# Performance work log

Hardware: AMD Instinct MI355X
Metric: run time of the kernel (lower is better)

The kernel has to match this reference:

```python
import jax, jax.numpy as jnp
import numpy as np

B, L, D = 32, 2048, 768
H = 512
EPS = 1e-5  # batch_norm eps (PyG MLP default norm)


def setup_inputs() -> dict:
    key = jax.random.key(0)
    ks = jax.random.split(key, 8)
    hidden = jax.random.normal(ks[0], (B, L, D), dtype=jnp.float32)
    attention_mask = jax.random.randint(ks[1], (B, L), 0, 2, dtype=jnp.int32)
    W1 = jax.random.normal(ks[2], (D, H), dtype=jnp.float32) * 0.02
    b1 = jnp.zeros((H,), dtype=jnp.float32)
    gamma = jnp.ones((H,), dtype=jnp.float32)
    beta = jnp.zeros((H,), dtype=jnp.float32)
    W2 = jax.random.normal(ks[3], (H, H), dtype=jnp.float32) * 0.02
    b2 = jnp.zeros((H,), dtype=jnp.float32)
    return {"hidden": hidden, "attention_mask": attention_mask,
            "W1": W1, "b1": b1, "gamma": gamma, "beta": beta,
            "W2": W2, "b2": b2}


def reference(hidden, attention_mask, W1, b1, gamma, beta, W2, b2):
    # Valid-token mask; pads are excluded from the batched graph's node set.
    m = attention_mask.astype(hidden.dtype)[..., None]  # (B, L, 1)
    n_valid = jnp.maximum(jnp.sum(m), 1.0)

    # MLP layer 1: Linear -> BatchNorm (stats over all valid nodes across the
    # whole batched graph, mirroring PyG MLP training-mode batch_norm) -> ReLU
    h = jnp.einsum('bld,dh->blh', hidden, W1) + b1  # (B, L, H)
    mean = jnp.sum(h * m, axis=(0, 1)) / n_valid
    var = jnp.sum(jnp.square(h - mean) * m, axis=(0, 1)) / n_valid
    h = (h - mean) * jax.lax.rsqrt(var + EPS) * gamma + beta
    h = jax.nn.relu(h)

    # MLP layer 2 (plain_last: no norm/act)
    out = jnp.einsum('blh,hk->blk', h, W2) + b2  # (B, L, H)

    # scores == ones -> segment softmax over each sequence's valid tokens is
    # uniform 1/n_b; scatter_add over batch ids == masked mean pool.
    counts = jnp.maximum(jnp.sum(m, axis=1), 1.0)  # (B, 1)
    pooled = jnp.sum(out * m, axis=1) / counts  # (B, H)
    return pooled
```

## Files before the change

### kernel.cpp

```cpp
#include <hip/hip_runtime.h>
#include <hip/hip_bf16.h>

#define Bn 32
#define Ln 2048
#define Dn 768
#define Hn 512
#define Mn (Bn*Ln)
#define EPSC 1e-5f

#define OFF_S1   0
#define OFF_S2   512
#define OFF_SC   1024
#define OFF_SH   1536
#define OFF_CNT  2048
#define OFF_PH   2304
#define ZERO_N   (OFF_PH + Bn*Hn)
#define OFF_W1T_BYTES  131072
#define OFF_H_BYTES    1048576

#define BM 128
#define BN2 256
#define BK 64
#define LDK 72

typedef __attribute__((ext_vector_type(8))) short bf16x8;
typedef __attribute__((ext_vector_type(4))) float f32x4;

static __device__ __forceinline__ unsigned short f2bf(float x) {
  __hip_bfloat16 h = __float2bfloat16(x);
  return *reinterpret_cast<unsigned short*>(&h);
}
static __device__ __forceinline__ float bf2f(unsigned short u) {
  return __uint_as_float(((unsigned int)u) << 16);
}

__global__ void zero_kernel(float* __restrict__ p, int n) {
  int i = blockIdx.x * 256 + threadIdx.x;
  if (i < n) p[i] = 0.f;
}

__global__ void count_kernel(const int* __restrict__ mask, float* __restrict__ cnt) {
  __shared__ int red[256];
  int b = blockIdx.x, t = threadIdx.x;
  int s = 0;
#pragma unroll
  for (int i = 0; i < 8; i++) s += mask[b * Ln + i * 256 + t];
  red[t] = s;
  __syncthreads();
  for (int off = 128; off > 0; off >>= 1) {
    if (t < off) red[t] += red[t + off];
    __syncthreads();
  }
  if (t == 0) cnt[b] = (float)red[0];
}

__global__ __launch_bounds__(256) void transpose_w1(
    const float* __restrict__ W1, unsigned short* __restrict__ W1t) {
  __shared__ float tile[32][33];
  int kx = blockIdx.x * 32;
  int nx = blockIdx.y * 32;
  int tx = threadIdx.x & 31, ty = threadIdx.x >> 5;
#pragma unroll
  for (int i = 0; i < 32; i += 8)
    tile[ty + i][tx] = W1[(size_t)(kx + ty + i) * Hn + nx + tx];
  __syncthreads();
#pragma unroll
  for (int i = 0; i < 32; i += 8)
    W1t[(size_t)(nx + ty + i) * Dn + kx + tx] = f2bf(tile[tx][ty + i]);
}

__global__ __launch_bounds__(512, 4) void gemm1_mfma(
    const float* __restrict__ A, const unsigned short* __restrict__ W1t,
    const float* __restrict__ b1, const int* __restrict__ mask,
    unsigned short* __restrict__ Hout,
    float* __restrict__ gsum, float* __restrict__ gsq)
{
  __shared__ unsigned short As[BM * LDK];
  __shared__ unsigned short Bs[BN2 * LDK];
  __shared__ float csum[BN2];
  __shared__ float csq[BN2];

  const int t = threadIdx.x;
  const int bx = blockIdx.x;
  const int by = blockIdx.y;
  const int bm0 = by * BM;
  const int bn0 = bx * BN2;

  const int w = t >> 6;
  const int lane = t & 63;
  const int wm0 = (w >> 2) * 64;
  const int wn0 = (w & 3) * 64;
  const int l15 = lane & 15;
  const int quad = lane >> 4;

  const int am = t >> 2;
  const int ak = (t & 3) * 16;
  const int bn = t >> 1;
  const int bk = (t & 1) * 32;

  const float* Ap = A + (size_t)(bm0 + am) * Dn + ak;
  const unsigned short* Bp = W1t + (size_t)(bn0 + bn) * Dn + bk;

  f32x4 acc[4][4];
#pragma unroll
  for (int i = 0; i < 4; i++)
#pragma unroll
    for (int j = 0; j < 4; j++) acc[i][j] = (f32x4){0.f, 0.f, 0.f, 0.f};

  for (int k0 = 0; k0 < Dn; k0 += BK) {
    float4 a0 = *(const float4*)(Ap + k0);
    float4 a1 = *(const float4*)(Ap + k0 + 4);
    float4 a2 = *(const float4*)(Ap + k0 + 8);
    float4 a3 = *(const float4*)(Ap + k0 + 12);
    uint4 bv0 = *(const uint4*)(Bp + k0);
    uint4 bv1 = *(const uint4*)(Bp + k0 + 8);
    uint4 bv2 = *(const uint4*)(Bp + k0 + 16);
    uint4 bv3 = *(const uint4*)(Bp + k0 + 24);
    __syncthreads();
    uint4 p0, p1;
    p0.x = (unsigned int)f2bf(a0.x) | ((unsigned int)f2bf(a0.y) << 16);
    p0.y = (unsigned int)f2bf(a0.z) | ((unsigned int)f2bf(a0.w) << 16);
    p0.z = (unsigned int)f2bf(a1.x) | ((unsigned int)f2bf(a1.y) << 16);
    p0.w = (unsigned int)f2bf(a1.z) | ((unsigned int)f2bf(a1.w) << 16);
    p1.x = (unsigned int)f2bf(a2.x) | ((unsigned int)f2bf(a2.y) << 16);
    p1.y = (unsigned int)f2bf(a2.z) | ((unsigned int)f2bf(a2.w) << 16);
    p1.z = (unsigned int)f2bf(a3.x) | ((unsigned int)f2bf(a3.y) << 16);
    p1.w = (unsigned int)f2bf(a3.z) | ((unsigned int)f2bf(a3.w) << 16);
    *(uint4*)&As[am * LDK + ak] = p0;
    *(uint4*)&As[am * LDK + ak + 8] = p1;
    *(uint4*)&Bs[bn * LDK + bk] = bv0;
    *(uint4*)&Bs[bn * LDK + bk + 8] = bv1;
    *(uint4*)&Bs[bn * LDK + bk + 16] = bv2;
    *(uint4*)&Bs[bn * LDK + bk + 24] = bv3;
    __syncthreads();
#pragma unroll
    for (int s = 0; s < 2; s++) {
      bf16x8 af[4], bf[4];
#pragma unroll
      for (int mt = 0; mt < 4; mt++)
        af[mt] = *(const bf16x8*)&As[(wm0 + mt * 16 + l15) * LDK + s * 32 + quad * 8];
#pragma unroll
      for (int nt = 0; nt < 4; nt++)
        bf[nt] = *(const bf16x8*)&Bs[(wn0 + nt * 16 + l15) * LDK + s * 32 + quad * 8];
#pragma unroll
      for (int mt = 0; mt < 4; mt++)
#pragma unroll
        for (int nt = 0; nt < 4; nt++)
          acc[mt][nt] = __builtin_amdgcn_mfma_f32_16x16x32_bf16(
              af[mt], bf[nt], acc[mt][nt], 0, 0, 0);
    }
  }

  if (t < BN2) { csum[t] = 0.f; csq[t] = 0.f; }
  __syncthreads();

  float mk[4][4];
#pragma unroll
  for (int mt = 0; mt < 4; mt++) {
    int4 mv = *(const int4*)(mask + bm0 + wm0 + mt * 16 + quad * 4);
    mk[mt][0] = (float)mv.x; mk[mt][1] = (float)mv.y;
    mk[mt][2] = (float)mv.z; mk[mt][3] = (float)mv.w;
  }

  const size_t cbase = ((size_t)(by * 2 + bx)) * 32768 + (size_t)w * 4096;
#pragma unroll
  for (int nt = 0; nt < 4; nt++) {
    const int nl = wn0 + nt * 16 + l15;
    const float bias = b1[bn0 + nl];
    float ps = 0.f, pq = 0.f;
#pragma unroll
    for (int mt = 0; mt < 4; mt++) {
      ushort4 st;
      float v0 = acc[mt][nt][0] + bias;
      float v1 = acc[mt][nt][1] + bias;
      float v2 = acc[mt][nt][2] + bias;
      float v3 = acc[mt][nt][3] + bias;
      ps += v0 * mk[mt][0] + v1 * mk[mt][1] + v2 * mk[mt][2] + v3 * mk[mt][3];
      pq += v0 * v0 * mk[mt][0] + v1 * v1 * mk[mt][1] +
            v2 * v2 * mk[mt][2] + v3 * v3 * mk[mt][3];
      st.x = f2bf(v0); st.y = f2bf(v1); st.z = f2bf(v2); st.w = f2bf(v3);
      *(ushort4*)&Hout[cbase + (size_t)(mt * 4 + nt) * 256 + lane * 4] = st;
    }
    atomicAdd(&csum[nl], ps);
    atomicAdd(&csq[nl], pq);
  }

  __syncthreads();
  if (t < BN2) {
    atomicAdd(&gsum[bn0 + t], csum[t]);
    atomicAdd(&gsq[bn0 + t], csq[t]);
  }
}

__global__ void finalize_kernel(float* __restrict__ ws,
                                const float* __restrict__ gamma,
                                const float* __restrict__ beta) {
  __shared__ float nv;
  int t = threadIdx.x;
  if (t == 0) {
    float s = 0.f;
    for (int i = 0; i < Bn; i++) s += ws[OFF_CNT + i];
    nv = fmaxf(s, 1.f);
  }
  __syncthreads();
  float inv = 1.f / nv;
  float m = ws[OFF_S1 + t] * inv;
  float var = ws[OFF_S2 + t] * inv - m * m;
  float istd = rsqrtf(fmaxf(var, 0.f) + EPSC);
  float sc = istd * gamma[t];
  ws[OFF_SC + t] = sc;
  ws[OFF_SH + t] = beta[t] - m * sc;
}

__global__ __launch_bounds__(256) void bnpool_kernel(
    const unsigned short* __restrict__ Hbuf, const int* __restrict__ mask,
    const float* __restrict__ sc, const float* __restrict__ sh,
    float* __restrict__ pooled)
{
  __shared__ float pool_c[BN2];
  __shared__ float mkf[BM];
  __shared__ float scs[BN2], shs[BN2];
  const int t = threadIdx.x;
  const int chunk = blockIdx.x;
  const int by = chunk >> 1, bx = chunk & 1;
  const int b = by >> 4;
  pool_c[t] = 0.f;
  if (t < BM) mkf[t] = (float)mask[by * BM + t];
  scs[t] = sc[bx * BN2 + t];
  shs[t] = sh[bx * BN2 + t];
  __syncthreads();
  const unsigned short* base = Hbuf + (size_t)chunk * 32768;
#pragma unroll 4
  for (int i = 0; i < 32; i++) {
    int o = (i * 256 + t) * 4;
    ushort4 hv = *(const ushort4*)(base + o);
    int lane = (o >> 2) & 63;
    int mtnt = (o >> 8) & 15;
    int w = o >> 12;
    int nl = (w & 3) * 64 + (mtnt & 3) * 16 + (lane & 15);
    int ml = (w >> 2) * 64 + (mtnt >> 2) * 16 + (lane >> 4) * 4;
    float4 mv = *(const float4*)&mkf[ml];
    float scv = scs[nl], shv = shs[nl];
    float s = 0.f;
    s = fmaf(fmaxf(fmaf(bf2f(hv.x), scv, shv), 0.f), mv.x, s);
    s = fmaf(fmaxf(fmaf(bf2f(hv.y), scv, shv), 0.f), mv.y, s);
    s = fmaf(fmaxf(fmaf(bf2f(hv.z), scv, shv), 0.f), mv.z, s);
    s = fmaf(fmaxf(fmaf(bf2f(hv.w), scv, shv), 0.f), mv.w, s);
    atomicAdd(&pool_c[nl], s);
  }
  __syncthreads();
  atomicAdd(&pooled[b * Hn + bx * BN2 + t], pool_c[t]);
}

__global__ __launch_bounds__(128) void final_kernel(
    const float* __restrict__ pooledh, const float* __restrict__ cnt,
    const float* __restrict__ W2, const float* __restrict__ b2,
    float* __restrict__ out)
{
  __shared__ float pr[Hn];
  int b = blockIdx.x >> 2;
  int cc = blockIdx.x & 3;
  int t = threadIdx.x;
  float nb = cnt[b];
  float inv = 1.f / fmaxf(nb, 1.f);
#pragma unroll
  for (int i = 0; i < 4; i++)
    pr[t + i * 128] = pooledh[b * Hn + t + i * 128] * inv;
  __syncthreads();
  int c = cc * 128 + t;
  float a = 0.f;
  for (int i = 0; i < Hn; i++)
    a = fmaf(pr[i], W2[(size_t)i * Hn + c], a);
  out[b * Hn + c] = a + b2[c] * (nb * inv);
}

extern "C" void kernel_launch(void* const* d_in, const int* in_sizes, int n_in,
                              void* d_out, int out_size, void* d_ws, size_t ws_size,
                              hipStream_t stream) {
  const float* hidden = (const float*)d_in[0];
  const int*   mask   = (const int*)d_in[1];
  const float* W1     = (const float*)d_in[2];
  const float* b1     = (const float*)d_in[3];
  const float* gamma  = (const float*)d_in[4];
  const float* beta   = (const float*)d_in[5];
  const float* W2     = (const float*)d_in[6];
  const float* b2     = (const float*)d_in[7];
  float* out = (float*)d_out;
  float* ws  = (float*)d_ws;
  unsigned short* W1t  = (unsigned short*)((char*)d_ws + OFF_W1T_BYTES);
  unsigned short* Hbuf = (unsigned short*)((char*)d_ws + OFF_H_BYTES);

  zero_kernel<<<(ZERO_N + 255) / 256, 256, 0, stream>>>(ws, ZERO_N);
  count_kernel<<<Bn, 256, 0, stream>>>(mask, ws + OFF_CNT);
  transpose_w1<<<dim3(Dn / 32, Hn / 32), 256, 0, stream>>>(W1, W1t);
  gemm1_mfma<<<dim3(Hn / BN2, Mn / BM), 512, 0, stream>>>(
      hidden, W1t, b1, mask, Hbuf, ws + OFF_S1, ws + OFF_S2);
  finalize_kernel<<<1, Hn, 0, stream>>>(ws, gamma, beta);
  bnpool_kernel<<<(Mn / BM) * (Hn / BN2), 256, 0, stream>>>(
      Hbuf, mask, ws + OFF_SC, ws + OFF_SH, ws + OFF_PH);
  final_kernel<<<Bn * 4, 128, 0, stream>>>(ws + OFF_PH, ws + OFF_CNT, W2, b2, out);
}
```

Measured before the change: 421.7 us.

## Prefetch GEMM tiles, store H column-major per chunk, atomic-free pooling per channel

Register-prefetches the next K slice of A and B in the GEMM main loop so global loads overlap the MFMA work. Changes the bf16 H intermediate layout to channel-major within each 128-row chunk, and rewrites the BN+ReLU+pool kernel to run one block per channel. Each block reduces all batches with warp shuffles and writes without atomics, which also lets the zeroing kernel skip the pooled buffer. The final matvec is split into four independent accumulators. Risks include higher register pressure in the GEMM and strided, less-coalesced reads in the pool kernel.

```diff
diff --git a/kernel.cpp b/kernel.cpp
--- a/kernel.cpp
+++ b/kernel.cpp
@@ -14,7 +14,7 @@
 #define OFF_SH   1536
 #define OFF_CNT  2048
 #define OFF_PH   2304
-#define ZERO_N   (OFF_PH + Bn*Hn)
+#define ZERO_N   1024
 #define OFF_W1T_BYTES  131072
 #define OFF_H_BYTES    1048576
 
@@ -107,32 +107,45 @@
 #pragma unroll
     for (int j = 0; j < 4; j++) acc[i][j] = (f32x4){0.f, 0.f, 0.f, 0.f};
 
+  float4 ra0 = *(const float4*)(Ap);
+  float4 ra1 = *(const float4*)(Ap + 4);
+  float4 ra2 = *(const float4*)(Ap + 8);
+  float4 ra3 = *(const float4*)(Ap + 12);
+  uint4 rb0 = *(const uint4*)(Bp);
+  uint4 rb1 = *(const uint4*)(Bp + 8);
+  uint4 rb2 = *(const uint4*)(Bp + 16);
+  uint4 rb3 = *(const uint4*)(Bp + 24);
+
   for (int k0 = 0; k0 < Dn; k0 += BK) {
-    float4 a0 = *(const float4*)(Ap + k0);
-    float4 a1 = *(const float4*)(Ap + k0 + 4);
-    float4 a2 = *(const float4*)(Ap + k0 + 8);
-    float4 a3 = *(const float4*)(Ap + k0 + 12);
-    uint4 bv0 = *(const uint4*)(Bp + k0);
-    uint4 bv1 = *(const uint4*)(Bp + k0 + 8);
-    uint4 bv2 = *(const uint4*)(Bp + k0 + 16);
-    uint4 bv3 = *(const uint4*)(Bp + k0 + 24);
     __syncthreads();
     uint4 p0, p1;
-    p0.x = (unsigned int)f2bf(a0.x) | ((unsigned int)f2bf(a0.y) << 16);
-    p0.y = (unsigned int)f2bf(a0.z) | ((unsigned int)f2bf(a0.w) << 16);
-    p0.z = (unsigned int)f2bf(a1.x) | ((unsigned int)f2bf(a1.y) << 16);
-    p0.w = (unsigned int)f2bf(a1.z) | ((unsigned int)f2bf(a1.w) << 16);
-    p1.x = (unsigned int)f2bf(a2.x) | ((unsigned int)f2bf(a2.y) << 16);
-    p1.y = (unsigned int)f2bf(a2.z) | ((unsigned int)f2bf(a2.w) << 16);
-    p1.z = (unsigned int)f2bf(a3.x) | ((unsigned int)f2bf(a3.y) << 16);
-    p1.w = (unsigned int)f2bf(a3.z) | ((unsigned int)f2bf(a3.w) << 16);
+    p0.x = (unsigned int)f2bf(ra0.x) | ((unsigned int)f2bf(ra0.y) << 16);
+    p0.y = (unsigned int)f2bf(ra0.z) | ((unsigned int)f2bf(ra0.w) << 16);
+    p0.z = (unsigned int)f2bf(ra1.x) | ((unsigned int)f2bf(ra1.y) << 16);
+    p0.w = (unsigned int)f2bf(ra1.z) | ((unsigned int)f2bf(ra1.w) << 16);
+    p1.x = (unsigned int)f2bf(ra2.x) | ((unsigned int)f2bf(ra2.y) << 16);
+    p1.y = (unsigned int)f2bf(ra2.z) | ((unsigned int)f2bf(ra2.w) << 16);
+    p1.z = (unsigned int)f2bf(ra3.x) | ((unsigned int)f2bf(ra3.y) << 16);
+    p1.w = (unsigned int)f2bf(ra3.z) | ((unsigned int)f2bf(ra3.w) << 16);
     *(uint4*)&As[am * LDK + ak] = p0;
     *(uint4*)&As[am * LDK + ak + 8] = p1;
-    *(uint4*)&Bs[bn * LDK + bk] = bv0;
-    *(uint4*)&Bs[bn * LDK + bk + 8] = bv1;
-    *(uint4*)&Bs[bn * LDK + bk + 16] = bv2;
-    *(uint4*)&Bs[bn * LDK + bk + 24] = bv3;
+    *(uint4*)&Bs[bn * LDK + bk] = rb0;
+    *(uint4*)&Bs[bn * LDK + bk + 8] = rb1;
+    *(uint4*)&Bs[bn * LDK + bk + 16] = rb2;
+    *(uint4*)&Bs[bn * LDK + bk + 24] = rb3;
     __syncthreads();
+
+    if (k0 + BK < Dn) {
+      ra0 = *(const float4*)(Ap + k0 + BK);
+      ra1 = *(const float4*)(Ap + k0 + BK + 4);
+      ra2 = *(const float4*)(Ap + k0 + BK + 8);
+      ra3 = *(const float4*)(Ap + k0 + BK + 12);
+      rb0 = *(const uint4*)(Bp + k0 + BK);
+      rb1 = *(const uint4*)(Bp + k0 + BK + 8);
+      rb2 = *(const uint4*)(Bp + k0 + BK + 16);
+      rb3 = *(const uint4*)(Bp + k0 + BK + 24);
+    }
+
 #pragma unroll
     for (int s = 0; s < 2; s++) {
       bf16x8 af[4], bf[4];
@@ -162,7 +175,7 @@
     mk[mt][2] = (float)mv.z; mk[mt][3] = (float)mv.w;
   }
 
-  const size_t cbase = ((size_t)(by * 2 + bx)) * 32768 + (size_t)w * 4096;
+  const size_t cbase = ((size_t)(by * 2 + bx)) * 32768;
 #pragma unroll
   for (int nt = 0; nt < 4; nt++) {
     const int nl = wn0 + nt * 16 + l15;
@@ -179,7 +192,7 @@
       pq += v0 * v0 * mk[mt][0] + v1 * v1 * mk[mt][1] +
             v2 * v2 * mk[mt][2] + v3 * v3 * mk[mt][3];
       st.x = f2bf(v0); st.y = f2bf(v1); st.z = f2bf(v2); st.w = f2bf(v3);
-      *(ushort4*)&Hout[cbase + (size_t)(mt * 4 + nt) * 256 + lane * 4] = st;
+      *(ushort4*)&Hout[cbase + (size_t)nl * 128 + wm0 + mt * 16 + quad * 4] = st;
     }
     atomicAdd(&csum[nl], ps);
     atomicAdd(&csq[nl], pq);
@@ -217,39 +230,41 @@
     const float* __restrict__ sc, const float* __restrict__ sh,
     float* __restrict__ pooled)
 {
-  __shared__ float pool_c[BN2];
-  __shared__ float mkf[BM];
-  __shared__ float scs[BN2], shs[BN2];
+  __shared__ float part[4][32];
   const int t = threadIdx.x;
-  const int chunk = blockIdx.x;
-  const int by = chunk >> 1, bx = chunk & 1;
-  const int b = by >> 4;
-  pool_c[t] = 0.f;
-  if (t < BM) mkf[t] = (float)mask[by * BM + t];
-  scs[t] = sc[bx * BN2 + t];
-  shs[t] = sh[bx * BN2 + t];
-  __syncthreads();
-  const unsigned short* base = Hbuf + (size_t)chunk * 32768;
+  const int c = blockIdx.x;
+  const int bx = c >> 8, cl = c & 255;
+  const int w4 = t >> 6, lane = t & 63;
+  const float scv = sc[c], shv = sh[c];
+
+  float acc[32];
+#pragma unroll
+  for (int j = 0; j < 32; j++) acc[j] = 0.f;
+
 #pragma unroll 4
-  for (int i = 0; i < 32; i++) {
-    int o = (i * 256 + t) * 4;
-    ushort4 hv = *(const ushort4*)(base + o);
-    int lane = (o >> 2) & 63;
-    int mtnt = (o >> 8) & 15;
-    int w = o >> 12;
-    int nl = (w & 3) * 64 + (mtnt & 3) * 16 + (lane & 15);
-    int ml = (w >> 2) * 64 + (mtnt >> 2) * 16 + (lane >> 4) * 4;
-    float4 mv = *(const float4*)&mkf[ml];
-    float scv = scs[nl], shv = shs[nl];
-    float s = 0.f;
-    s = fmaf(fmaxf(fmaf(bf2f(hv.x), scv, shv), 0.f), mv.x, s);
-    s = fmaf(fmaxf(fmaf(bf2f(hv.y), scv, shv), 0.f), mv.y, s);
-    s = fmaf(fmaxf(fmaf(bf2f(hv.z), scv, shv), 0.f), mv.z, s);
-    s = fmaf(fmaxf(fmaf(bf2f(hv.w), scv, shv), 0.f), mv.w, s);
-    atomicAdd(&pool_c[nl], s);
-  }
-  __syncthreads();
-  atomicAdd(&pooled[b * Hn + bx * BN2 + t], pool_c[t]);
+  for (int jj = 0; jj < 32; jj++) {
+#pragma unroll
+    for (int s = 0; s < 4; s++) {
+      const int by = jj * 16 + s * 4 + w4;
+      const size_t base = ((size_t)(by * 2 + bx)) * 32768 + (size_t)cl * 128;
+      unsigned int hv = *(const unsigned int*)(Hbuf + base + lane * 2);
+      int2 mv = *(const int2*)(mask + by * 128 + lane * 2);
+      float v0 = fmaxf(fmaf(bf2f((unsigned short)hv), scv, shv), 0.f);
+      float v1 = fmaxf(fmaf(bf2f((unsigned short)(hv >> 16)), scv, shv), 0.f);
+      acc[jj] += v0 * (float)mv.x + v1 * (float)mv.y;
+    }
+  }
+
+#pragma unroll
+  for (int j = 0; j < 32; j++) {
+    float v = acc[j];
+#pragma unroll
+    for (int off = 32; off > 0; off >>= 1) v += __shfl_down(v, off);
+    if (lane == 0) part[w4][j] = v;
+  }
+  __syncthreads();
+  if (t < 32)
+    pooled[t * Hn + c] = part[0][t] + part[1][t] + part[2][t] + part[3][t];
 }
 
 __global__ __launch_bounds__(128) void final_kernel(
@@ -268,10 +283,14 @@
     pr[t + i * 128] = pooledh[b * Hn + t + i * 128] * inv;
   __syncthreads();
   int c = cc * 128 + t;
-  float a = 0.f;
-  for (int i = 0; i < Hn; i++)
-    a = fmaf(pr[i], W2[(size_t)i * Hn + c], a);
-  out[b * Hn + c] = a + b2[c] * (nb * inv);
+  float a0 = 0.f, a1 = 0.f, a2 = 0.f, a3 = 0.f;
+  for (int i = 0; i < Hn; i += 4) {
+    a0 = fmaf(pr[i],     W2[(size_t)i * Hn + c],           a0);
+    a1 = fmaf(pr[i + 1], W2[(size_t)(i + 1) * Hn + c],     a1);
+    a2 = fmaf(pr[i + 2], W2[(size_t)(i + 2) * Hn + c],     a2);
+    a3 = fmaf(pr[i + 3], W2[(size_t)(i + 3) * Hn + c],     a3);
+  }
+  out[b * Hn + c] = (a0 + a1) + (a2 + a3) + b2[c] * (nb * inv);
 }
 
 extern "C" void kernel_launch(void* const* d_in, const int* in_sizes, int n_in,
@@ -296,7 +315,7 @@
   gemm1_mfma<<<dim3(Hn / BN2, Mn / BM), 512, 0, stream>>>(
       hidden, W1t, b1, mask, Hbuf, ws + OFF_S1, ws + OFF_S2);
   finalize_kernel<<<1, Hn, 0, stream>>>(ws, gamma, beta);
-  bnpool_kernel<<<(Mn / BM) * (Hn / BN2), 256, 0, stream>>>(
+  bnpool_kernel<<<Hn, 256, 0, stream>>>(
       Hbuf, mask, ws + OFF_SC, ws + OFF_SH, ws + OFF_PH);
   final_kernel<<<Bn * 4, 128, 0, stream>>>(ws + OFF_PH, ws + OFF_CNT, W2, b2, out);
 }
```

New measurement: 444.5 us. 1.05x slower.
